# Kernel tuning notes

Measured on AMD Instinct MI355X. Metric: run time of the kernel, lower is better.

The kernel has to match this reference:

```python
import jax, jax.numpy as jnp
import numpy as np

N, NPG, BS = 32000, 1000, 32
E, H, L, R, K = 512000, 128, 3, 8, 64


def setup_inputs() -> dict:
    key = jax.random.key(0)
    ks = jax.random.split(key, 16)
    sc = 0.05
    x = jax.random.normal(ks[0], (N, H), jnp.float32)
    W_rel = jax.random.normal(ks[1], (L, R, H, H), jnp.float32) * sc
    W_self = jax.random.normal(ks[2], (L, H, H), jnp.float32) * sc
    rel_table = jax.random.normal(ks[3], (R, H), jnp.float32)
    Zn = jax.random.normal(ks[4], (K, H), jnp.float32) * sc
    proj_W = jax.random.normal(ks[5], (L * H, H), jnp.float32) * sc
    proj_b = jnp.zeros((H,), jnp.float32)
    fc_W = jax.random.normal(ks[6], (2 * L * H + 2 * H, 1), jnp.float32) * sc
    fc_b = jnp.zeros((1,), jnp.float32)
    rep_seq = jax.random.normal(ks[7], (BS, H), jnp.float32)
    src = jax.random.randint(ks[8], (E,), 0, N, jnp.int32)
    dst = jax.random.randint(ks[9], (E,), 0, N, jnp.int32)
    etype = jax.random.randint(ks[10], (E,), 0, R, jnp.int32)
    graph_id = (jnp.arange(N, dtype=jnp.int32) // NPG).astype(jnp.int32)
    head_ids = (jnp.arange(BS, dtype=jnp.int32) * NPG)           # node with id==1 per subgraph
    tail_ids = (jnp.arange(BS, dtype=jnp.int32) * NPG + 1)       # node with id==2 per subgraph
    rel_labels = jax.random.randint(ks[11], (BS,), 0, R, jnp.int32)
    return dict(x=x, W_rel=W_rel, W_self=W_self, rel_table=rel_table, Zn=Zn,
                proj_W=proj_W, proj_b=proj_b, fc_W=fc_W, fc_b=fc_b, rep_seq=rep_seq,
                src=src, dst=dst, etype=etype, graph_id=graph_id,
                head_ids=head_ids, tail_ids=tail_ids, rel_labels=rel_labels)


def reference(x, W_rel, W_self, rel_table, Zn, proj_W, proj_b, fc_W, fc_b, rep_seq,
              src, dst, etype, graph_id, head_ids, tail_ids, rel_labels):
    n, h_dim = x.shape
    bs = head_ids.shape[0]
    # RGCN message passing: aggregate src features per (dst, rel), then per-rel linear.
    seg = dst.astype(jnp.int32) * R + etype.astype(jnp.int32)  # [E]
    h = x
    reprs = []
    for l in range(L):
        agg = jax.ops.segment_sum(h[src], seg, num_segments=n * R)  # [N*R, H]
        agg = agg.reshape(n, R, h_dim)
        msg = jnp.einsum('nri,rio->no', agg, W_rel[l])
        h = jax.nn.relu(msg + h @ W_self[l])
        reprs.append(h)
    repr_ = jnp.stack(reprs, axis=1)  # [N, L, H]
    # mean_nodes pooling per subgraph
    counts = jax.ops.segment_sum(jnp.ones((n,), x.dtype), graph_id, num_segments=bs)
    g_mean = jax.ops.segment_sum(repr_, graph_id, num_segments=bs) / counts[:, None, None]
    g_out = jax.nn.leaky_relu(g_mean.reshape(bs, L * h_dim) @ proj_W + proj_b)  # [bs, H]
    # head/tail gathers
    head_flat = repr_[head_ids].reshape(bs, L * h_dim)
    tail_flat = repr_[tail_ids].reshape(bs, L * h_dim)
    rel_embs = rel_table[rel_labels]  # [bs, H]
    h_out = head_flat @ proj_W + proj_b
    t_out = tail_flat @ proj_W + proj_b
    # community view: cluster assignment (softmax) then summary (sigmoid)
    s1 = jax.nn.sigmoid(jax.nn.softmax(h_out @ Zn.T, axis=-1) @ Zn)
    s2 = jax.nn.sigmoid(jax.nn.softmax(t_out @ Zn.T, axis=-1) @ Zn)
    s = s1 * s2
    # view attention aggregation over [subgraph, sequence, community] views
    views = jnp.stack([g_out, rep_seq, s], axis=1)  # [bs, 3, H]
    att = jax.nn.softmax(jnp.sum(rel_embs[:, None, :] * views, axis=-1), axis=-1)  # [bs, 3]
    view_aggr = jnp.sum(att[:, :, None] * views, axis=1)  # [bs, H]
    # positive triplet scoring
    g_rep = jnp.concatenate([head_flat, tail_flat, rel_embs, view_aggr], axis=1)
    out_pos = g_rep @ fc_W + fc_b  # [bs, 1]
    return out_pos
```

## Files before the change

kernel.cpp:

```cpp
#include <hip/hip_runtime.h>

#define N_NODES 32000
#define NPG     1000
#define BSZ     32
#define NEDGE   512000
#define H       128
#define NL      3
#define NR      8
#define NW      1152
#define NBIN2   262144

typedef __attribute__((ext_vector_type(8))) short short8;
typedef __attribute__((ext_vector_type(4))) float float4v;

__device__ __forceinline__ float bf2f(unsigned short u) {
  union { unsigned int i; float f; } v;
  v.i = ((unsigned int)u) << 16;
  return v.f;
}
__device__ __forceinline__ unsigned short f2bf(float f) {
  union { float f; unsigned int i; } v;
  v.f = f;
  unsigned int x = v.i;
  return (unsigned short)((x + 0x7FFFu + ((x >> 16) & 1u)) >> 16);
}

__global__ __launch_bounds__(256) void k_prep(
    const float* __restrict__ x, const float* __restrict__ W_rel,
    const float* __restrict__ W_self, const int* __restrict__ dst,
    const int* __restrict__ graph_id,
    unsigned short* __restrict__ hb, unsigned short* __restrict__ Bt,
    int* __restrict__ cnt, int* __restrict__ gcount)
{
  const int b = blockIdx.x, t = threadIdx.x;
  if (b < 4000) {
    const size_t i = ((size_t)b * 256 + t) * 4;
    float4 v = *(const float4*)(x + i);
    ushort4 u = { f2bf(v.x), f2bf(v.y), f2bf(v.z), f2bf(v.w) };
    *(ushort4*)(hb + i) = u;
  } else if (b < 5728) {
    const int g = (b - 4000) * 256 + t;
    const int k = g & 127;
    const int n = (g >> 7) % NW;
    const int l = g / (NW * H);
    float v = (n < 1024) ? W_rel[(((size_t)l * NR + (n >> 7)) * H + k) * H + (n & 127)]
                         : W_self[((size_t)l * H + k) * H + (n - 1024)];
    Bt[(size_t)l * (NW * H) + (size_t)n * H + k] = f2bf(v);
  } else if (b < 7728) {
    const int bb = b - 5728;
    const int e = bb * 256 + t;
    atomicAdd(&cnt[dst[e] * 8 + (bb & 7)], 1);
  } else {
    __shared__ int hist[BSZ];
    if (t < BSZ) hist[t] = 0;
    __syncthreads();
    const int n = (b - 7728) * 256 + t;
    if (n < N_NODES) atomicAdd(&hist[graph_id[n]], 1);
    __syncthreads();
    if (t < BSZ) { int v = hist[t]; if (v) atomicAdd(&gcount[t], v); }
  }
}

__global__ __launch_bounds__(256) void k_scanA(const int* __restrict__ cnt,
                                               int* __restrict__ bsum) {
  __shared__ int red[256];
  const int t = threadIdx.x;
  int4 v = *(const int4*)(cnt + blockIdx.x * 1024 + t * 4);
  red[t] = v.x + v.y + v.z + v.w;
  __syncthreads();
  for (int off = 128; off > 0; off >>= 1) {
    if (t < off) red[t] += red[t + off];
    __syncthreads();
  }
  if (t == 0) bsum[blockIdx.x] = red[0];
}

__global__ __launch_bounds__(256) void k_scanB(const int* __restrict__ bsum,
                                               int* __restrict__ boff) {
  __shared__ int v[256];
  const int t = threadIdx.x;
  v[t] = bsum[t];
  __syncthreads();
  if (t == 0) {
    int r = 0;
    for (int i = 0; i < 256; ++i) { int c = v[i]; v[i] = r; r += c; }
  }
  __syncthreads();
  boff[t] = v[t];
}

__global__ __launch_bounds__(256) void k_scanC(const int* __restrict__ cnt,
                                               const int* __restrict__ boff,
                                               int* __restrict__ row_ptr2,
                                               int* __restrict__ cursor) {
  __shared__ int ts[256];
  const int t = threadIdx.x;
  const int base = blockIdx.x * 1024 + t * 4;
  int4 v = *(const int4*)(cnt + base);
  const int s = v.x + v.y + v.z + v.w;
  ts[t] = s;
  __syncthreads();
  for (int off = 1; off < 256; off <<= 1) {
    int val = (t >= off) ? ts[t - off] : 0;
    __syncthreads();
    ts[t] += val;
    __syncthreads();
  }
  int ex = ts[t] - s + boff[blockIdx.x];
  int4 w = { ex, ex + v.x, ex + v.x + v.y, ex + v.x + v.y + v.z };
  *(int4*)(row_ptr2 + base) = w;
  *(int4*)(cursor + base) = w;
}

__global__ void k_fill(const int* __restrict__ src, const int* __restrict__ dst,
                       const int* __restrict__ etype, int* __restrict__ cursor,
                       int* __restrict__ edge_off) {
  int e = blockIdx.x * blockDim.x + threadIdx.x;
  if (e < NEDGE) {
    int p = atomicAdd(&cursor[dst[e] * 8 + (blockIdx.x & 7)], 1);
    edge_off[p] = src[e] * NW + etype[e] * H;
  }
}

__global__ __launch_bounds__(256) void k_gemm9(
    const unsigned short* __restrict__ Ah,
    const unsigned short* __restrict__ Bt,
    unsigned short* __restrict__ G)
{
  __shared__ unsigned short lds_a[128 * 136];
  __shared__ unsigned short lds_b[128 * 136];
  const int tid  = threadIdx.x;
  const int wave = tid >> 6, lane = tid & 63;
  const int l15 = lane & 15, quad = lane >> 4;
  const int m0 = blockIdx.x * 128;
  const int n0 = blockIdx.y * 128;
  const int mb = (wave & 1) * 64;
  const int nb = (wave >> 1) * 64;

  #pragma unroll
  for (int s = 0; s < 8; ++s) {
    int f  = s * 256 + tid;
    int m  = f >> 4;
    int ko = (f & 15) * 8;
    *(uint4*)(lds_a + m * 136 + ko) = *(const uint4*)(Ah + (size_t)(m0 + m) * H + ko);
    *(uint4*)(lds_b + m * 136 + ko) = *(const uint4*)(Bt + (size_t)(n0 + m) * H + ko);
  }
  __syncthreads();

  float4v acc[4][4];
  #pragma unroll
  for (int i = 0; i < 4; ++i)
    #pragma unroll
    for (int j = 0; j < 4; ++j) acc[i][j] = (float4v){0.f, 0.f, 0.f, 0.f};

  #pragma unroll
  for (int ks = 0; ks < 4; ++ks) {
    const int ko = ks * 32 + quad * 8;
    short8 afr[4], bfr[4];
    #pragma unroll
    for (int i = 0; i < 4; ++i)
      afr[i] = *(const short8*)(lds_a + (mb + i * 16 + l15) * 136 + ko);
    #pragma unroll
    for (int j = 0; j < 4; ++j)
      bfr[j] = *(const short8*)(lds_b + (nb + j * 16 + l15) * 136 + ko);
    #pragma unroll
    for (int i = 0; i < 4; ++i)
      #pragma unroll
      for (int j = 0; j < 4; ++j)
        acc[i][j] = __builtin_amdgcn_mfma_f32_16x16x32_bf16(afr[i], bfr[j], acc[i][j], 0, 0, 0);
  }

  __syncthreads();
  #pragma unroll
  for (int i = 0; i < 4; ++i)
    #pragma unroll
    for (int j = 0; j < 4; ++j)
      #pragma unroll
      for (int r = 0; r < 4; ++r)
        lds_a[(mb + i * 16 + quad * 4 + r) * 136 + nb + j * 16 + l15] = f2bf(acc[i][j][r]);
  __syncthreads();
  #pragma unroll
  for (int s = 0; s < 8; ++s) {
    int f  = s * 256 + tid;
    int m  = f >> 4;
    int ko = (f & 15) * 8;
    *(uint4*)(G + (size_t)(m0 + m) * NW + n0 + ko) = *(const uint4*)(lds_a + m * 136 + ko);
  }
}

__global__ __launch_bounds__(256) void k_gather(
    const unsigned short* __restrict__ G, const int* __restrict__ row_ptr2,
    const int* __restrict__ edge_off, unsigned short* __restrict__ Hnext)
{
  const int node = blockIdx.x * 4 + (threadIdx.x >> 6);
  const int lane = threadIdx.x & 63;
  const int half = lane >> 5;
  const int li   = lane & 31;
  const int c0   = li * 4;
  const int beg = row_ptr2[node << 3];
  const int end = row_ptr2[(node << 3) + 8];
  float s0 = 0.f, s1 = 0.f, s2 = 0.f, s3 = 0.f;
  if (half == 0) {
    uint2 u = *(const uint2*)(G + (size_t)node * NW + 1024 + c0);
    s0 = bf2f((unsigned short)(u.x & 0xffff));
    s1 = bf2f((unsigned short)(u.x >> 16));
    s2 = bf2f((unsigned short)(u.y & 0xffff));
    s3 = bf2f((unsigned short)(u.y >> 16));
  }
#define ACC4(u) { \
    s0 += bf2f((unsigned short)((u).x & 0xffff)); \
    s1 += bf2f((unsigned short)((u).x >> 16));    \
    s2 += bf2f((unsigned short)((u).y & 0xffff)); \
    s3 += bf2f((unsigned short)((u).y >> 16)); }
  int e = beg + half;
  for (; e + 6 < end; e += 8) {
    int o0 = edge_off[e],     o1 = edge_off[e + 2];
    int o2 = edge_off[e + 4], o3 = edge_off[e + 6];
    uint2 u0 = *(const uint2*)(G + o0 + c0);
    uint2 u1 = *(const uint2*)(G + o1 + c0);
    uint2 u2 = *(const uint2*)(G + o2 + c0);
    uint2 u3 = *(const uint2*)(G + o3 + c0);
    ACC4(u0) ACC4(u1) ACC4(u2) ACC4(u3)
  }
  for (; e < end; e += 2) {
    int o = edge_off[e];
    uint2 u = *(const uint2*)(G + o + c0);
    ACC4(u)
  }
#undef ACC4
  s0 += __shfl_xor(s0, 32);
  s1 += __shfl_xor(s1, 32);
  s2 += __shfl_xor(s2, 32);
  s3 += __shfl_xor(s3, 32);
  if (half == 0) {
    uint2 w;
    w.x = (unsigned int)f2bf(fmaxf(s0, 0.f)) | ((unsigned int)f2bf(fmaxf(s1, 0.f)) << 16);
    w.y = (unsigned int)f2bf(fmaxf(s2, 0.f)) | ((unsigned int)f2bf(fmaxf(s3, 0.f)) << 16);
    *(uint2*)(Hnext + (size_t)node * H + c0) = w;
  }
}

__global__ void k_gmean(const unsigned short* __restrict__ hb, float* __restrict__ gmean)
{
  const int g = blockIdx.x, l = blockIdx.y, c = blockIdx.z, t = threadIdx.x;
  const unsigned short* base =
      hb + ((size_t)(l + 1) * N_NODES + (size_t)g * NPG + (size_t)c * (NPG / 8)) * H + t * 2;
  float sx = 0.f, sy = 0.f;
  for (int i = 0; i < 125; ++i) {
    unsigned int u = *(const unsigned int*)(base + (size_t)i * H);
    sx += bf2f((unsigned short)(u & 0xffff));
    sy += bf2f((unsigned short)(u >> 16));
  }
  float* gp = gmean + (size_t)g * (NL * H) + l * H + t * 2;
  atomicAdd(gp, sx);
  atomicAdd(gp + 1, sy);
}

__global__ __launch_bounds__(128) void k_final(
    const unsigned short* __restrict__ hb, const float* __restrict__ gmean,
    const int* __restrict__ gcount,
    const float* __restrict__ rel_tb, const float* __restrict__ Zn,
    const float* __restrict__ projW, const float* __restrict__ projB,
    const float* __restrict__ fcW, const float* __restrict__ fcB,
    const float* __restrict__ repSeq,
    const int* __restrict__ head_ids, const int* __restrict__ tail_ids,
    const int* __restrict__ rel_lab, float* __restrict__ out)
{
  const int b = blockIdx.x;
  const int o = threadIdx.x;
  __shared__ float gm[384], hf[384], tf[384];
  __shared__ float go[128], ho[128], t_o[128], re[128], rs[128], sv[128];
  __shared__ float lg[128], pr[128], red[128], att[3];

  const int hid = head_ids[b], tlid = tail_ids[b], rl = rel_lab[b];
  const float cinv = 1.f / (float)gcount[b];
  #pragma unroll
  for (int l = 0; l < NL; ++l) {
    gm[l * H + o] = gmean[(size_t)b * (NL * H) + l * H + o] * cinv;
    hf[l * H + o] = bf2f(hb[((size_t)(l + 1) * N_NODES + hid) * H + o]);
    tf[l * H + o] = bf2f(hb[((size_t)(l + 1) * N_NODES + tlid) * H + o]);
  }
  re[o] = rel_tb[rl * H + o];
  rs[o] = repSeq[b * H + o];
  __syncthreads();

  float pb = projB[o];
  float sg = pb, sh = pb, st = pb;
  for (int i = 0; i < NL * H; ++i) {
    float wv = projW[i * H + o];
    sg = fmaf(gm[i], wv, sg);
    sh = fmaf(hf[i], wv, sh);
    st = fmaf(tf[i], wv, st);
  }
  go[o] = (sg > 0.f) ? sg : 0.01f * sg;
  ho[o] = sh;
  t_o[o] = st;
  __syncthreads();

  {
    const int k = o & 63;
    const float* v = (o < 64) ? ho : t_o;
    float s = 0.f;
    for (int i = 0; i < H; ++i) s = fmaf(v[i], Zn[k * H + i], s);
    lg[o] = s;
  }
  __syncthreads();
  if (o < 2) {
    float* l0 = &lg[o * 64];
    float* p0 = &pr[o * 64];
    float mx = l0[0];
    for (int k = 1; k < 64; ++k) mx = fmaxf(mx, l0[k]);
    float sum = 0.f;
    for (int k = 0; k < 64; ++k) { float e = __expf(l0[k] - mx); p0[k] = e; sum += e; }
    float inv = 1.f / sum;
    for (int k = 0; k < 64; ++k) p0[k] *= inv;
  }
  __syncthreads();
  {
    float s1 = 0.f, s2 = 0.f;
    for (int k = 0; k < 64; ++k) {
      float z = Zn[k * H + o];
      s1 = fmaf(pr[k], z, s1);
      s2 = fmaf(pr[64 + k], z, s2);
    }
    s1 = 1.f / (1.f + __expf(-s1));
    s2 = 1.f / (1.f + __expf(-s2));
    sv[o] = s1 * s2;
  }
  __syncthreads();
  if (o == 0) {
    float d0 = 0.f, d1 = 0.f, d2 = 0.f;
    for (int i = 0; i < H; ++i) { d0 += re[i] * go[i]; d1 += re[i] * rs[i]; d2 += re[i] * sv[i]; }
    float mx = fmaxf(d0, fmaxf(d1, d2));
    float e0 = __expf(d0 - mx), e1 = __expf(d1 - mx), e2 = __expf(d2 - mx);
    float inv = 1.f / (e0 + e1 + e2);
    att[0] = e0 * inv; att[1] = e1 * inv; att[2] = e2 * inv;
  }
  __syncthreads();
  float va = att[0] * go[o] + att[1] * rs[o] + att[2] * sv[o];

  float p = 0.f;
  p = fmaf(hf[o],       fcW[o],       p);
  p = fmaf(hf[128 + o], fcW[128 + o], p);
  p = fmaf(hf[256 + o], fcW[256 + o], p);
  p = fmaf(tf[o],       fcW[384 + o], p);
  p = fmaf(tf[128 + o], fcW[512 + o], p);
  p = fmaf(tf[256 + o], fcW[640 + o], p);
  p = fmaf(re[o],       fcW[768 + o], p);
  p = fmaf(va,          fcW[896 + o], p);
  red[o] = p;
  __syncthreads();
  if (o == 0) {
    float s = 0.f;
    for (int i = 0; i < 128; ++i) s += red[i];
    out[b] = s + fcB[0];
  }
}

extern "C" void kernel_launch(void* const* d_in, const int* in_sizes, int n_in,
                              void* d_out, int out_size, void* d_ws, size_t ws_size,
                              hipStream_t stream) {
  const float* x        = (const float*)d_in[0];
  const float* W_rel    = (const float*)d_in[1];
  const float* W_self   = (const float*)d_in[2];
  const float* rel_tb   = (const float*)d_in[3];
  const float* Zn       = (const float*)d_in[4];
  const float* proj_W   = (const float*)d_in[5];
  const float* proj_b   = (const float*)d_in[6];
  const float* fc_W     = (const float*)d_in[7];
  const float* fc_b     = (const float*)d_in[8];
  const float* rep_seq  = (const float*)d_in[9];
  const int* src      = (const int*)d_in[10];
  const int* dst      = (const int*)d_in[11];
  const int* etype    = (const int*)d_in[12];
  const int* graph_id = (const int*)d_in[13];
  const int* head_ids = (const int*)d_in[14];
  const int* tail_ids = (const int*)d_in[15];
  const int* rel_lab  = (const int*)d_in[16];
  float* out = (float*)d_out;

  char* w = (char*)d_ws;
  unsigned short* G  = (unsigned short*)w; w += (size_t)N_NODES * NW * 2;
  unsigned short* hb = (unsigned short*)w; w += (size_t)(NL + 1) * N_NODES * H * 2;
  unsigned short* Bt = (unsigned short*)w; w += (size_t)NL * NW * H * 2;
  int* row_ptr2 = (int*)w;  w += (size_t)(NBIN2 + 8) * 4;
  int* cursor   = (int*)w;  w += (size_t)NBIN2 * 4;
  int* edge_off = (int*)w;  w += (size_t)NEDGE * 4;
  int* bsum     = (int*)w;  w += (size_t)256 * 4;
  int* boff     = (int*)w;  w += (size_t)256 * 4;
  char* z = w;
  int* cnt     = (int*)w;   w += (size_t)NBIN2 * 4;
  int* gcount  = (int*)w;   w += (size_t)32 * 4;
  float* gmean = (float*)w; w += (size_t)BSZ * NL * H * 4;
  size_t zbytes = (size_t)(w - z);

  hipMemsetAsync(z, 0, zbytes, stream);
  k_prep <<<7853, 256, 0, stream>>>(x, W_rel, W_self, dst, graph_id, hb, Bt, cnt, gcount);
  k_scanA<<<NBIN2 / 1024, 256, 0, stream>>>(cnt, bsum);
  k_scanB<<<1, 256, 0, stream>>>(bsum, boff);
  k_scanC<<<NBIN2 / 1024, 256, 0, stream>>>(cnt, boff, row_ptr2, cursor);
  k_fill <<<NEDGE / 256, 256, 0, stream>>>(src, dst, etype, cursor, edge_off);

  for (int l = 0; l < NL; ++l) {
    const unsigned short* hp = hb + (size_t)l * N_NODES * H;
    unsigned short* hn = hb + (size_t)(l + 1) * N_NODES * H;
    k_gemm9 <<<dim3(N_NODES / 128, 9), 256, 0, stream>>>(hp, Bt + (size_t)l * NW * H, G);
    k_gather<<<N_NODES / 4, 256, 0, stream>>>(G, row_ptr2, edge_off, hn);
  }
  k_gmean<<<dim3(BSZ, NL, 8), 64, 0, stream>>>(hb, gmean);
  k_final<<<BSZ, H, 0, stream>>>(hb, gmean, gcount, rel_tb, Zn, proj_W, proj_b, fc_W, fc_b,
                                 rep_seq, head_ids, tail_ids, rel_lab, out);
  (void)in_sizes; (void)n_in; (void)out_size; (void)ws_size;
}
```

Measured before the change: 342.6 us.

## Aggregate then transform: fuse per-relation gather with GEMM per layer

```diff
diff --git a/kernel.cpp b/kernel.cpp
--- a/kernel.cpp
+++ b/kernel.cpp
@@ -7,7 +7,8 @@
 #define H       128
 #define NL      3
 #define NR      8
-#define NW      1152
+#define NKK     1152
+#define ASTR    1160
 #define NBIN2   262144
 
 typedef __attribute__((ext_vector_type(8))) short short8;
@@ -28,7 +29,7 @@
 __global__ __launch_bounds__(256) void k_prep(
     const float* __restrict__ x, const float* __restrict__ W_rel,
     const float* __restrict__ W_self, const int* __restrict__ dst,
-    const int* __restrict__ graph_id,
+    const int* __restrict__ etype, const int* __restrict__ graph_id,
     unsigned short* __restrict__ hb, unsigned short* __restrict__ Bt,
     int* __restrict__ cnt, int* __restrict__ gcount)
 {
@@ -40,16 +41,17 @@
     *(ushort4*)(hb + i) = u;
   } else if (b < 5728) {
     const int g = (b - 4000) * 256 + t;
-    const int k = g & 127;
-    const int n = (g >> 7) % NW;
-    const int l = g / (NW * H);
-    float v = (n < 1024) ? W_rel[(((size_t)l * NR + (n >> 7)) * H + k) * H + (n & 127)]
-                         : W_self[((size_t)l * H + k) * H + (n - 1024)];
-    Bt[(size_t)l * (NW * H) + (size_t)n * H + k] = f2bf(v);
+    const int l = g / (H * NKK);
+    const int rem = g - l * (H * NKK);
+    const int o = rem / NKK;
+    const int kk = rem - o * NKK;
+    float v = (kk < 1024)
+        ? W_rel[(((size_t)l * NR + (kk >> 7)) * H + (kk & 127)) * H + o]
+        : W_self[((size_t)l * H + (kk - 1024)) * H + o];
+    Bt[g] = f2bf(v);
   } else if (b < 7728) {
-    const int bb = b - 5728;
-    const int e = bb * 256 + t;
-    atomicAdd(&cnt[dst[e] * 8 + (bb & 7)], 1);
+    const int e = (b - 5728) * 256 + t;
+    atomicAdd(&cnt[dst[e] * 8 + etype[e]], 1);
   } else {
     __shared__ int hist[BSZ];
     if (t < BSZ) hist[t] = 0;
@@ -75,38 +77,27 @@
   if (t == 0) bsum[blockIdx.x] = red[0];
 }
 
-__global__ __launch_bounds__(256) void k_scanB(const int* __restrict__ bsum,
-                                               int* __restrict__ boff) {
-  __shared__ int v[256];
-  const int t = threadIdx.x;
-  v[t] = bsum[t];
-  __syncthreads();
-  if (t == 0) {
-    int r = 0;
-    for (int i = 0; i < 256; ++i) { int c = v[i]; v[i] = r; r += c; }
-  }
-  __syncthreads();
-  boff[t] = v[t];
-}
-
 __global__ __launch_bounds__(256) void k_scanC(const int* __restrict__ cnt,
-                                               const int* __restrict__ boff,
+                                               const int* __restrict__ bsum,
                                                int* __restrict__ row_ptr2,
                                                int* __restrict__ cursor) {
-  __shared__ int ts[256];
+  __shared__ int ts[256], bsx[256];
   const int t = threadIdx.x;
   const int base = blockIdx.x * 1024 + t * 4;
   int4 v = *(const int4*)(cnt + base);
   const int s = v.x + v.y + v.z + v.w;
-  ts[t] = s;
+  ts[t]  = s;
+  bsx[t] = bsum[t];
   __syncthreads();
   for (int off = 1; off < 256; off <<= 1) {
-    int val = (t >= off) ? ts[t - off] : 0;
-    __syncthreads();
-    ts[t] += val;
-    __syncthreads();
-  }
-  int ex = ts[t] - s + boff[blockIdx.x];
+    int a = (t >= off) ? ts[t - off]  : 0;
+    int c = (t >= off) ? bsx[t - off] : 0;
+    __syncthreads();
+    ts[t] += a; bsx[t] += c;
+    __syncthreads();
+  }
+  const int boff = (blockIdx.x == 0) ? 0 : bsx[blockIdx.x - 1];
+  int ex = ts[t] - s + boff;
   int4 w = { ex, ex + v.x, ex + v.x + v.y, ex + v.x + v.y + v.z };
   *(int4*)(row_ptr2 + base) = w;
   *(int4*)(cursor + base) = w;
@@ -117,126 +108,98 @@
                        int* __restrict__ edge_off) {
   int e = blockIdx.x * blockDim.x + threadIdx.x;
   if (e < NEDGE) {
-    int p = atomicAdd(&cursor[dst[e] * 8 + (blockIdx.x & 7)], 1);
-    edge_off[p] = src[e] * NW + etype[e] * H;
-  }
-}
-
-__global__ __launch_bounds__(256) void k_gemm9(
-    const unsigned short* __restrict__ Ah,
-    const unsigned short* __restrict__ Bt,
-    unsigned short* __restrict__ G)
+    int p = atomicAdd(&cursor[dst[e] * 8 + etype[e]], 1);
+    edge_off[p] = src[e];
+  }
+}
+
+__global__ __launch_bounds__(256, 2) void k_layer(
+    const unsigned short* __restrict__ Hin,
+    const unsigned short* __restrict__ Bt2,
+    const int* __restrict__ row_ptr2,
+    const int* __restrict__ edge_off,
+    unsigned short* __restrict__ Hout)
 {
-  __shared__ unsigned short lds_a[128 * 136];
-  __shared__ unsigned short lds_b[128 * 136];
+  __shared__ unsigned short A_sh[32 * ASTR];
   const int tid  = threadIdx.x;
-  const int wave = tid >> 6, lane = tid & 63;
-  const int l15 = lane & 15, quad = lane >> 4;
-  const int m0 = blockIdx.x * 128;
-  const int n0 = blockIdx.y * 128;
-  const int mb = (wave & 1) * 64;
-  const int nb = (wave >> 1) * 64;
+  const int wv   = tid >> 6, lane = tid & 63;
+  const int half = lane >> 5, li = lane & 31;
+  const int l15  = lane & 15, quad = lane >> 4;
+  const int n0   = blockIdx.x * 32;
+  const unsigned int* Hu = (const unsigned int*)Hin;
+
+  for (int batch = 0; batch < 8; ++batch) {
+    const int nl = batch * 4 + wv;
+    const int n  = n0 + nl;
+    const int rb = n * 8 + half * 4;
+    int eb[4], ee[4];
+    eb[0] = row_ptr2[rb + 0];
+    eb[1] = row_ptr2[rb + 1];
+    eb[2] = row_ptr2[rb + 2];
+    eb[3] = row_ptr2[rb + 3];
+    ee[0] = eb[1]; ee[1] = eb[2]; ee[2] = eb[3];
+    ee[3] = row_ptr2[rb + 4];
+    int steps = max(max(ee[0] - eb[0], ee[1] - eb[1]),
+                    max(ee[2] - eb[2], ee[3] - eb[3]));
+    float acc[4][4] = {};
+    for (int it = 0; it < steps; ++it) {
+      #pragma unroll
+      for (int s = 0; s < 4; ++s) {
+        const int e = eb[s] + it;
+        const bool ok = e < ee[s];
+        const int idx = ok ? e : 0;
+        const int srcn = edge_off[idx];
+        uint2 u = *(const uint2*)(Hu + (size_t)srcn * 64 + li * 2);
+        const unsigned int ux = ok ? u.x : 0u;
+        const unsigned int uy = ok ? u.y : 0u;
+        acc[s][0] += bf2f((unsigned short)(ux & 0xffff));
+        acc[s][1] += bf2f((unsigned short)(ux >> 16));
+        acc[s][2] += bf2f((unsigned short)(uy & 0xffff));
+        acc[s][3] += bf2f((unsigned short)(uy >> 16));
+      }
+    }
+    #pragma unroll
+    for (int s = 0; s < 4; ++s) {
+      ushort4 w4 = { f2bf(acc[s][0]), f2bf(acc[s][1]), f2bf(acc[s][2]), f2bf(acc[s][3]) };
+      *(ushort4*)(A_sh + nl * ASTR + (half * 4 + s) * H + li * 4) = w4;
+    }
+    *(unsigned int*)(A_sh + nl * ASTR + 1024 + lane * 2) = Hu[(size_t)n * 64 + lane];
+  }
+  __syncthreads();
+
+  float4v c00 = {0.f,0.f,0.f,0.f}, c01 = {0.f,0.f,0.f,0.f};
+  float4v c10 = {0.f,0.f,0.f,0.f}, c11 = {0.f,0.f,0.f,0.f};
+  const unsigned short* Bw = Bt2 + (size_t)(wv * 32) * NKK;
+  #pragma unroll 4
+  for (int ks = 0; ks < 36; ++ks) {
+    const int kk = ks * 32 + quad * 8;
+    short8 a0 = *(const short8*)(A_sh + l15 * ASTR + kk);
+    short8 a1 = *(const short8*)(A_sh + (16 + l15) * ASTR + kk);
+    short8 b0 = *(const short8*)(Bw + (size_t)l15 * NKK + kk);
+    short8 b1 = *(const short8*)(Bw + (size_t)(16 + l15) * NKK + kk);
+    c00 = __builtin_amdgcn_mfma_f32_16x16x32_bf16(a0, b0, c00, 0, 0, 0);
+    c01 = __builtin_amdgcn_mfma_f32_16x16x32_bf16(a0, b1, c01, 0, 0, 0);
+    c10 = __builtin_amdgcn_mfma_f32_16x16x32_bf16(a1, b0, c10, 0, 0, 0);
+    c11 = __builtin_amdgcn_mfma_f32_16x16x32_bf16(a1, b1, c11, 0, 0, 0);
+  }
+  __syncthreads();
 
   #pragma unroll
-  for (int s = 0; s < 8; ++s) {
-    int f  = s * 256 + tid;
-    int m  = f >> 4;
-    int ko = (f & 15) * 8;
-    *(uint4*)(lds_a + m * 136 + ko) = *(const uint4*)(Ah + (size_t)(m0 + m) * H + ko);
-    *(uint4*)(lds_b + m * 136 + ko) = *(const uint4*)(Bt + (size_t)(n0 + m) * H + ko);
-  }
-  __syncthreads();
-
-  float4v acc[4][4];
+  for (int r = 0; r < 4; ++r) {
+    const int row0 = quad * 4 + r, row1 = 16 + quad * 4 + r;
+    const int col0 = wv * 32 + l15, col1 = wv * 32 + 16 + l15;
+    A_sh[row0 * 136 + col0] = f2bf(fmaxf(c00[r], 0.f));
+    A_sh[row0 * 136 + col1] = f2bf(fmaxf(c01[r], 0.f));
+    A_sh[row1 * 136 + col0] = f2bf(fmaxf(c10[r], 0.f));
+    A_sh[row1 * 136 + col1] = f2bf(fmaxf(c11[r], 0.f));
+  }
+  __syncthreads();
   #pragma unroll
-  for (int i = 0; i < 4; ++i)
-    #pragma unroll
-    for (int j = 0; j < 4; ++j) acc[i][j] = (float4v){0.f, 0.f, 0.f, 0.f};
-
-  #pragma unroll
-  for (int ks = 0; ks < 4; ++ks) {
-    const int ko = ks * 32 + quad * 8;
-    short8 afr[4], bfr[4];
-    #pragma unroll
-    for (int i = 0; i < 4; ++i)
-      afr[i] = *(const short8*)(lds_a + (mb + i * 16 + l15) * 136 + ko);
-    #pragma unroll
-    for (int j = 0; j < 4; ++j)
-      bfr[j] = *(const short8*)(lds_b + (nb + j * 16 + l15) * 136 + ko);
-    #pragma unroll
-    for (int i = 0; i < 4; ++i)
-      #pragma unroll
-      for (int j = 0; j < 4; ++j)
-        acc[i][j] = __builtin_amdgcn_mfma_f32_16x16x32_bf16(afr[i], bfr[j], acc[i][j], 0, 0, 0);
-  }
-
-  __syncthreads();
-  #pragma unroll
-  for (int i = 0; i < 4; ++i)
-    #pragma unroll
-    for (int j = 0; j < 4; ++j)
-      #pragma unroll
-      for (int r = 0; r < 4; ++r)
-        lds_a[(mb + i * 16 + quad * 4 + r) * 136 + nb + j * 16 + l15] = f2bf(acc[i][j][r]);
-  __syncthreads();
-  #pragma unroll
-  for (int s = 0; s < 8; ++s) {
-    int f  = s * 256 + tid;
-    int m  = f >> 4;
-    int ko = (f & 15) * 8;
-    *(uint4*)(G + (size_t)(m0 + m) * NW + n0 + ko) = *(const uint4*)(lds_a + m * 136 + ko);
-  }
-}
-
-__global__ __launch_bounds__(256) void k_gather(
-    const unsigned short* __restrict__ G, const int* __restrict__ row_ptr2,
-    const int* __restrict__ edge_off, unsigned short* __restrict__ Hnext)
-{
-  const int node = blockIdx.x * 4 + (threadIdx.x >> 6);
-  const int lane = threadIdx.x & 63;
-  const int half = lane >> 5;
-  const int li   = lane & 31;
-  const int c0   = li * 4;
-  const int beg = row_ptr2[node << 3];
-  const int end = row_ptr2[(node << 3) + 8];
-  float s0 = 0.f, s1 = 0.f, s2 = 0.f, s3 = 0.f;
-  if (half == 0) {
-    uint2 u = *(const uint2*)(G + (size_t)node * NW + 1024 + c0);
-    s0 = bf2f((unsigned short)(u.x & 0xffff));
-    s1 = bf2f((unsigned short)(u.x >> 16));
-    s2 = bf2f((unsigned short)(u.y & 0xffff));
-    s3 = bf2f((unsigned short)(u.y >> 16));
-  }
-#define ACC4(u) { \
-    s0 += bf2f((unsigned short)((u).x & 0xffff)); \
-    s1 += bf2f((unsigned short)((u).x >> 16));    \
-    s2 += bf2f((unsigned short)((u).y & 0xffff)); \
-    s3 += bf2f((unsigned short)((u).y >> 16)); }
-  int e = beg + half;
-  for (; e + 6 < end; e += 8) {
-    int o0 = edge_off[e],     o1 = edge_off[e + 2];
-    int o2 = edge_off[e + 4], o3 = edge_off[e + 6];
-    uint2 u0 = *(const uint2*)(G + o0 + c0);
-    uint2 u1 = *(const uint2*)(G + o1 + c0);
-    uint2 u2 = *(const uint2*)(G + o2 + c0);
-    uint2 u3 = *(const uint2*)(G + o3 + c0);
-    ACC4(u0) ACC4(u1) ACC4(u2) ACC4(u3)
-  }
-  for (; e < end; e += 2) {
-    int o = edge_off[e];
-    uint2 u = *(const uint2*)(G + o + c0);
-    ACC4(u)
-  }
-#undef ACC4
-  s0 += __shfl_xor(s0, 32);
-  s1 += __shfl_xor(s1, 32);
-  s2 += __shfl_xor(s2, 32);
-  s3 += __shfl_xor(s3, 32);
-  if (half == 0) {
-    uint2 w;
-    w.x = (unsigned int)f2bf(fmaxf(s0, 0.f)) | ((unsigned int)f2bf(fmaxf(s1, 0.f)) << 16);
-    w.y = (unsigned int)f2bf(fmaxf(s2, 0.f)) | ((unsigned int)f2bf(fmaxf(s3, 0.f)) << 16);
-    *(uint2*)(Hnext + (size_t)node * H + c0) = w;
+  for (int rep = 0; rep < 2; ++rep) {
+    const int ch = rep * 256 + tid;
+    const int node = ch >> 4, c = ch & 15;
+    *(uint4*)(Hout + (size_t)(n0 + node) * H + c * 8) =
+        *(const uint4*)(A_sh + node * 136 + c * 8);
   }
 }
 
@@ -380,14 +343,12 @@
   float* out = (float*)d_out;
 
   char* w = (char*)d_ws;
-  unsigned short* G  = (unsigned short*)w; w += (size_t)N_NODES * NW * 2;
-  unsigned short* hb = (unsigned short*)w; w += (size_t)(NL + 1) * N_NODES * H * 2;
-  unsigned short* Bt = (unsigned short*)w; w += (size_t)NL * NW * H * 2;
+  unsigned short* hb  = (unsigned short*)w; w += (size_t)(NL + 1) * N_NODES * H * 2;
+  unsigned short* Bt2 = (unsigned short*)w; w += (size_t)NL * H * NKK * 2;
   int* row_ptr2 = (int*)w;  w += (size_t)(NBIN2 + 8) * 4;
   int* cursor   = (int*)w;  w += (size_t)NBIN2 * 4;
   int* edge_off = (int*)w;  w += (size_t)NEDGE * 4;
   int* bsum     = (int*)w;  w += (size_t)256 * 4;
-  int* boff     = (int*)w;  w += (size_t)256 * 4;
   char* z = w;
   int* cnt     = (int*)w;   w += (size_t)NBIN2 * 4;
   int* gcount  = (int*)w;   w += (size_t)32 * 4;
@@ -395,17 +356,16 @@
   size_t zbytes = (size_t)(w - z);
 
   hipMemsetAsync(z, 0, zbytes, stream);
-  k_prep <<<7853, 256, 0, stream>>>(x, W_rel, W_self, dst, graph_id, hb, Bt, cnt, gcount);
+  k_prep <<<7853, 256, 0, stream>>>(x, W_rel, W_self, dst, etype, graph_id, hb, Bt2, cnt, gcount);
   k_scanA<<<NBIN2 / 1024, 256, 0, stream>>>(cnt, bsum);
-  k_scanB<<<1, 256, 0, stream>>>(bsum, boff);
-  k_scanC<<<NBIN2 / 1024, 256, 0, stream>>>(cnt, boff, row_ptr2, cursor);
+  k_scanC<<<NBIN2 / 1024, 256, 0, stream>>>(cnt, bsum, row_ptr2, cursor);
   k_fill <<<NEDGE / 256, 256, 0, stream>>>(src, dst, etype, cursor, edge_off);
 
   for (int l = 0; l < NL; ++l) {
     const unsigned short* hp = hb + (size_t)l * N_NODES * H;
     unsigned short* hn = hb + (size_t)(l + 1) * N_NODES * H;
-    k_gemm9 <<<dim3(N_NODES / 128, 9), 256, 0, stream>>>(hp, Bt + (size_t)l * NW * H, G);
-    k_gather<<<N_NODES / 4, 256, 0, stream>>>(G, row_ptr2, edge_off, hn);
+    k_layer<<<N_NODES / 32, 256, 0, stream>>>(hp, Bt2 + (size_t)l * H * NKK,
+                                              row_ptr2, edge_off, hn);
   }
   k_gmean<<<dim3(BSZ, NL, 8), 64, 0, stream>>>(hb, gmean);
   k_final<<<BSZ, H, 0, stream>>>(hb, gmean, gcount, rel_tb, Zn, proj_W, proj_b, fc_W, fc_b,
```

After: 478.5 us. 39.7% more time.
